# Kernel optimization log

Hardware: AMD Instinct MI355X
Metric: run time of the kernel (lower is better)

Reference implementation:

```python
import jax, jax.numpy as jnp
import numpy as np

D_MODEL = 2048
NUM_HEADS = 16
D_K = D_MODEL // NUM_HEADS


def setup_inputs() -> dict:
    key = jax.random.key(0)
    ks = jax.random.split(key, 9)
    s = 1.0 / np.sqrt(D_MODEL)
    x = jax.random.normal(ks[0], (4, 4096, D_MODEL), dtype=jnp.float32)
    wq = jax.random.uniform(ks[1], (D_MODEL, D_MODEL), jnp.float32, -s, s)
    bq = jax.random.uniform(ks[2], (D_MODEL,), jnp.float32, -s, s)
    wk = jax.random.uniform(ks[3], (D_MODEL, D_MODEL), jnp.float32, -s, s)
    bk = jax.random.uniform(ks[4], (D_MODEL,), jnp.float32, -s, s)
    wv = jax.random.uniform(ks[5], (D_MODEL, D_MODEL), jnp.float32, -s, s)
    bv = jax.random.uniform(ks[6], (D_MODEL,), jnp.float32, -s, s)
    wo = jax.random.uniform(ks[7], (D_MODEL, D_MODEL), jnp.float32, -s, s)
    bo = jax.random.uniform(ks[8], (D_MODEL,), jnp.float32, -s, s)
    return {"x": x, "wq": wq, "bq": bq, "wk": wk, "bk": bk,
            "wv": wv, "bv": bv, "wo": wo, "bo": bo}


def _heads(t, B, S):
    # (B, S, d_model) -> (B, H, S, d_k)
    return t.reshape(B, S, NUM_HEADS, D_K).transpose(0, 2, 1, 3)


def reference(x, wq, bq, wk, bk, wv, bv, wo, bo):
    B, S, _ = x.shape
    Q = _heads(x @ wq.T + bq, B, S)
    K = _heads(x @ wk.T + bk, B, S)
    V = _heads(x @ wv.T + bv, B, S)
    # elu(x)+1 feature map
    Q = jax.nn.elu(Q) + 1.0
    K = jax.nn.elu(K) + 1.0
    # KV: (B,H,d_k,d_k)
    KV = jnp.einsum('bhsd,bhse->bhde', K, V)
    QKV = jnp.einsum('bhsd,bhde->bhse', Q, KV)
    K_sum = jnp.sum(K, axis=-2)                      # (B,H,d_k)
    QK_sum = jnp.einsum('bhsd,bhd->bhs', Q, K_sum)   # (B,H,S)
    out = QKV / (QK_sum[..., None] + 1e-8)
    out = out.transpose(0, 2, 1, 3).reshape(B, S, D_MODEL)
    return out @ wo.T + bo
```

## Files before the change

kernel.cpp:

```cpp
#include <hip/hip_runtime.h>


#define D_MODEL 2048
#define SEQ     4096
#define BATCH   4
#define HEADS   16
#define DKH     128
#define M_TOK   16384
#define NBH     64

using frag8 = __attribute__((ext_vector_type(8))) short;
using f32x4 = __attribute__((ext_vector_type(4))) float;

typedef __attribute__((address_space(1))) const unsigned int g_u32;
typedef __attribute__((address_space(3))) unsigned int       l_u32;

__device__ __forceinline__ unsigned short f2bf(float f) {
  unsigned u = __float_as_uint(f);
  u = u + 0x7fffu + ((u >> 16) & 1u);
  return (unsigned short)(u >> 16);
}
__device__ __forceinline__ float bf2f(unsigned short h) {
  return __uint_as_float(((unsigned)h) << 16);
}

__global__ __launch_bounds__(256) void convert_f2bf_kernel(
    const float* __restrict__ in, unsigned short* __restrict__ out, int n4) {
  int i = blockIdx.x * 256 + threadIdx.x;
  if (i < n4) {
    float4 v = reinterpret_cast<const float4*>(in)[i];
    ushort4 o;
    o.x = f2bf(v.x); o.y = f2bf(v.y); o.z = f2bf(v.z); o.w = f2bf(v.w);
    reinterpret_cast<ushort4*>(out)[i] = o;
  }
}


#define ST_B(GB, LD, SLOT, KC)                                                \
  _Pragma("unroll") for (int j_ = 0; j_ < 2; ++j_)                            \
    __builtin_amdgcn_global_load_lds(                                         \
        (g_u32*)((GB) + (srow + wid * 16 + j_ * 8 + (lane >> 3)) * (LD)       \
                 + (KC) + scg * 8),                                           \
        (l_u32*)(sh + (SLOT) * 16384 + 8192 + (wid * 16 + j_ * 8) * 64),      \
        16, 0, 0);

#define ST_A(GA, LD, SP, ST, KC)                                              \
    __builtin_amdgcn_global_load_lds(                                         \
        (g_u32*)((GA) + (srow + (ST) * 32 + (wid & 3) * 8 + (lane >> 3)) * (LD) \
                 + (KC) + (wid >> 2) * 32 + scg * 8),                         \
        (l_u32*)(sh + ((SP) + (wid >> 2)) * 16384 +                           \
                 ((ST) * 32 + (wid & 3) * 8) * 64),                           \
        16, 0, 0);

#define RD_A(S0, S1, Q)                                                       \
  a0[0] = *(const frag8*)(lds + (S0) * 16384 + tA + (Q) * 2048);              \
  a0[1] = *(const frag8*)(lds + (S0) * 16384 + tA + (Q) * 2048 + 1024);       \
  a1[0] = *(const frag8*)(lds + (S1) * 16384 + tA + (Q) * 2048);              \
  a1[1] = *(const frag8*)(lds + (S1) * 16384 + tA + (Q) * 2048 + 1024);

#define RD_B(D0, D1, S0, S1)                                                  \
  _Pragma("unroll") for (int n_ = 0; n_ < 4; ++n_) {                          \
    D0[n_] = *(const frag8*)(lds + (S0) * 16384 + tB + n_ * 1024);            \
    D1[n_] = *(const frag8*)(lds + (S1) * 16384 + tB + n_ * 1024);            \
  }

#define MM8(AQ, B0, B1)                                                       \
  __builtin_amdgcn_s_setprio(1);                                              \
  _Pragma("unroll") for (int j_ = 0; j_ < 2; ++j_)                            \
  _Pragma("unroll") for (int n_ = 0; n_ < 4; ++n_)                            \
    acc[(AQ) + j_][n_] = __builtin_amdgcn_mfma_f32_16x16x32_bf16(             \
        a0[j_], B0[n_], acc[(AQ) + j_][n_], 0, 0, 0);                         \
  _Pragma("unroll") for (int j_ = 0; j_ < 2; ++j_)                            \
  _Pragma("unroll") for (int n_ = 0; n_ < 4; ++n_)                            \
    acc[(AQ) + j_][n_] = __builtin_amdgcn_mfma_f32_16x16x32_bf16(             \
        a1[j_], B1[n_], acc[(AQ) + j_][n_], 0, 0, 0);                         \
  __builtin_amdgcn_s_setprio(0);

#define BAR __builtin_amdgcn_s_barrier()
#define LG0                                                                   \
  asm volatile("s_waitcnt lgkmcnt(0)" ::: "memory");                          \
  __builtin_amdgcn_sched_barrier(0)

template <int MODE, bool XMAJOR>
__global__ __launch_bounds__(512, 2) void gemm256_nt_kernel(
    const unsigned short* __restrict__ A, long lda,
    const unsigned short* __restrict__ Bm, long ldb,
    void* __restrict__ Cv, long ldc,
    const float* __restrict__ bias, float* __restrict__ aux, int K) {
  __shared__ unsigned short sh[65536];
  const int lane = threadIdx.x & 63, wid = threadIdx.x >> 6;
  const int wm = wid >> 2, wn = wid & 3;
  const int lr = lane & 15, lh = lane >> 4;

  const int gx = gridDim.x, gy = gridDim.y;
  const int cpx = (gx * gy) >> 3;
  const int P = blockIdx.y * gx + blockIdx.x;
  const int Lw = (P & 7) * cpx + (P >> 3);
  int bx, by;
  if (XMAJOR) { bx = Lw / gy; by = Lw - bx * gy; }
  else        { by = Lw / gx; bx = Lw - by * gx; }

  const long m0 = (long)by * 256, n0 = (long)bx * 256;
  const unsigned short* Ablk = A + m0 * lda;
  const unsigned short* Bblk = Bm + n0 * ldb;
  const int NT = K >> 6;

  const int qA = (wm * 4 + lh) ^ (lr & 7);
  const int qB = ((wn >> 1) * 4 + lh) ^ (lr & 7);
  const unsigned short* lds = sh;
  const int tA = lr * 64 + qA * 8;
  const int tB = 8192 + ((wn & 1) * 64 + lr) * 64 + qB * 8;

  const int sqd = (lane & 7) ^ (lane >> 3);
  const int scg = sqd & 3;
  const long srow = (long)((sqd >> 2) * 128);

  f32x4 acc[8][4];
#pragma unroll
  for (int m = 0; m < 8; ++m)
#pragma unroll
    for (int n = 0; n < 4; ++n) acc[m][n] = (f32x4){0.f, 0.f, 0.f, 0.f};

  frag8 a0[2], a1[2], bu0[4], bu1[4], bv0[4], bv1[4];

  ST_B(Bblk, ldb, 0, 0)
  ST_B(Bblk, ldb, 1, 32)
  ST_A(Ablk, lda, 0, 0, 0) ST_A(Ablk, lda, 0, 1, 0)
  ST_A(Ablk, lda, 0, 2, 0) ST_A(Ablk, lda, 0, 3, 0)
  if (NT > 1) {
    ST_B(Bblk, ldb, 2, 64)
    ST_B(Bblk, ldb, 3, 96)
    ST_A(Ablk, lda, 2, 0, 64) ST_A(Ablk, lda, 2, 1, 64)
  }
  asm volatile("s_waitcnt vmcnt(6)" ::: "memory");
  BAR;

  const int NI = NT >> 1;
  for (int i = 0; i < NI; ++i) {
    const int kv = i * 128 + 64, kw = i * 128 + 128, kx = i * 128 + 192;
    const bool wok = (i + 1) < NI;
    RD_A(0, 1, 0)
    RD_B(bu0, bu1, 0, 1)
    ST_A(Ablk, lda, 2, 2, kv) ST_A(Ablk, lda, 2, 3, kv)
    asm volatile("s_waitcnt lgkmcnt(8)" ::: "memory");
    BAR; LG0;
    MM8(0, bu0, bu1)
    BAR;
    RD_A(0, 1, 1)
    if (wok) { ST_B(Bblk, ldb, 0, kw) }
    BAR; LG0;
    MM8(2, bu0, bu1)
    BAR;
    RD_A(0, 1, 2)
    if (wok) { ST_B(Bblk, ldb, 1, kw + 32) }
    BAR; LG0;
    MM8(4, bu0, bu1)
    BAR;
    RD_A(0, 1, 3)
    if (wok) { ST_A(Ablk, lda, 0, 0, kw) ST_A(Ablk, lda, 0, 1, kw) }
    if (wok) asm volatile("s_waitcnt vmcnt(6)" ::: "memory");
    else     asm volatile("s_waitcnt vmcnt(0)" ::: "memory");
    BAR; LG0;
    MM8(6, bu0, bu1)
    BAR;
    RD_A(2, 3, 0)
    RD_B(bv0, bv1, 2, 3)
    if (wok) { ST_A(Ablk, lda, 0, 2, kw) ST_A(Ablk, lda, 0, 3, kw) }
    asm volatile("s_waitcnt lgkmcnt(8)" ::: "memory");
    BAR; LG0;
    MM8(0, bv0, bv1)
    BAR;
    RD_A(2, 3, 1)
    if (wok) { ST_B(Bblk, ldb, 2, kx) }
    BAR; LG0;
    MM8(2, bv0, bv1)
    BAR;
    RD_A(2, 3, 2)
    if (wok) { ST_B(Bblk, ldb, 3, kx + 32) }
    BAR; LG0;
    MM8(4, bv0, bv1)
    BAR;
    RD_A(2, 3, 3)
    if (wok) { ST_A(Ablk, lda, 2, 0, kx) ST_A(Ablk, lda, 2, 1, kx)
               asm volatile("s_waitcnt vmcnt(6)" ::: "memory"); }
    BAR; LG0;
    MM8(6, bv0, bv1)
    BAR;
  }

  if constexpr (MODE == 1) {
    __shared__ float red2[256];
    if (threadIdx.x < 256) red2[threadIdx.x] = 0.f;
    __syncthreads();
#pragma unroll
    for (int m = 0; m < 8; ++m)
#pragma unroll
      for (int r = 0; r < 4; ++r) {
        const int lrow = wm * 128 + (m >> 1) * 32 + (m & 1) * 16 + lh * 4 + r;
        const long row = m0 + lrow;
        float part = 0.f;
#pragma unroll
        for (int n = 0; n < 4; ++n) {
          long col = n0 + wn * 64 + n * 16 + lr;
          float v = acc[m][n][r] + bias[row];
          v = v > 0.f ? v + 1.f : __expf(v);
          unsigned short us = f2bf(v);
          ((unsigned short*)Cv)[row * ldc + col] = us;
          part += bf2f(us);
        }
#pragma unroll
        for (int s = 1; s < 16; s <<= 1) part += __shfl_xor(part, s);
        if (lr == 0) atomicAdd(&red2[lrow], part);
      }
    __syncthreads();
    if (threadIdx.x < 256)
      atomicAdd(&aux[(n0 >> 12) * 2048 + m0 + threadIdx.x], red2[threadIdx.x]);
  } else {
#pragma unroll
    for (int m = 0; m < 8; ++m)
#pragma unroll
      for (int n = 0; n < 4; ++n)
#pragma unroll
        for (int r = 0; r < 4; ++r) {
          long row = m0 + wm * 128 + (m >> 1) * 32 + (m & 1) * 16 + lh * 4 + r;
          long col = n0 + wn * 64 + n * 16 + lr;
          float v = acc[m][n][r];
          if (MODE == 0) {
            v += bias[col]; v = v > 0.f ? v + 1.f : __expf(v);
            ((unsigned short*)Cv)[row * ldc + col] = f2bf(v);
          } else if (MODE == 2) {
            v += bias[row];
            ((unsigned short*)Cv)[row * ldc + col] = f2bf(v);
          } else {
            v += bias[col];
            ((float*)Cv)[row * ldc + col] = v;
          }
        }
  }
}

__device__ __forceinline__ void stage_tile(const unsigned short* __restrict__ G,
                                           long ld, unsigned short* __restrict__ L) {
  const int w = threadIdx.x >> 6, l = threadIdx.x & 63;
#pragma unroll
  for (int r = 0; r < 4; ++r) {
    const int chunk = w * 4 + r;
    const int row = chunk * 8 + (l >> 3);
    const int col = (l & 7) * 8;
    __builtin_amdgcn_global_load_lds((g_u32*)(G + (long)row * ld + col),
                                     (l_u32*)(L + chunk * 512), 16, 0, 0);
  }
}

__device__ __forceinline__ void gemm_mainloop(const unsigned short* __restrict__ A, long lda,
                                              const unsigned short* __restrict__ B, long ldb,
                                              int K, unsigned short* lA, unsigned short* lB,
                                              f32x4 acc[4][4]) {
  const int lane = threadIdx.x & 63;
  const int wid  = threadIdx.x >> 6;
  const int wr = wid >> 1, wc = wid & 1;
  const int lr = lane & 15, lh = lane >> 4;
  for (int k0 = 0; k0 < K; k0 += 64) {
    stage_tile(A + k0, lda, lA);
    stage_tile(B + k0, ldb, lB);
    __syncthreads();
#pragma unroll
    for (int kk = 0; kk < 64; kk += 32) {
      frag8 av[4], bv[4];
#pragma unroll
      for (int m = 0; m < 4; ++m)
        av[m] = *reinterpret_cast<const frag8*>(lA + (wr * 64 + m * 16 + lr) * 64 + kk + lh * 8);
#pragma unroll
      for (int n = 0; n < 4; ++n)
        bv[n] = *reinterpret_cast<const frag8*>(lB + (wc * 64 + n * 16 + lr) * 64 + kk + lh * 8);
#pragma unroll
      for (int m = 0; m < 4; ++m)
#pragma unroll
        for (int n = 0; n < 4; ++n)
          acc[m][n] = __builtin_amdgcn_mfma_f32_16x16x32_bf16(av[m], bv[n], acc[m][n], 0, 0, 0);
    }
    __syncthreads();
  }
}

#define ACC_INIT(acc)                                   \
  _Pragma("unroll") for (int m_ = 0; m_ < 4; ++m_)      \
  _Pragma("unroll") for (int n_ = 0; n_ < 4; ++n_)      \
      acc[m_][n_] = (f32x4){0.f, 0.f, 0.f, 0.f};

__global__ __launch_bounds__(256) void kvt_partial_kernel(
    const unsigned short* __restrict__ VT, const unsigned short* __restrict__ KT,
    float* __restrict__ part) {
  __shared__ unsigned short lA[128 * 64], lB[128 * 64];
  const int z = blockIdx.x;
  const int bh = z >> 3, c = z & 7;
  const int b = bh >> 4, h = bh & 15;
  const long tOff = (long)b * SEQ + (long)c * 512;
  const unsigned short* A  = VT + (long)(h * DKH) * M_TOK + tOff;
  const unsigned short* Bm = KT + (long)(h * DKH) * M_TOK + tOff;
  f32x4 acc[4][4];
  ACC_INIT(acc);
  gemm_mainloop(A, M_TOK, Bm, M_TOK, 512, lA, lB, acc);
  const int lane = threadIdx.x & 63, wid = threadIdx.x >> 6;
  const int wr = wid >> 1, wc = wid & 1, lr = lane & 15, lh = lane >> 4;
  float* out = part + (long)z * (DKH * DKH);
#pragma unroll
  for (int m = 0; m < 4; ++m)
#pragma unroll
    for (int n = 0; n < 4; ++n)
#pragma unroll
      for (int r = 0; r < 4; ++r) {
        int row = wr * 64 + m * 16 + lh * 4 + r;
        int col = wc * 64 + n * 16 + lr;
        out[row * DKH + col] = acc[m][n][r];
      }
}

__global__ __launch_bounds__(256) void reduce_kvt_kernel(
    const float* __restrict__ part, unsigned short* __restrict__ kvt) {
  int i = blockIdx.x * 256 + threadIdx.x;
  if (i < NBH * DKH * DKH) {
    int bh = i >> 14, j = i & 16383;
    float s = 0.f;
#pragma unroll
    for (int c = 0; c < 8; ++c) s += part[(((long)bh * 8 + c) << 14) + j];
    kvt[i] = f2bf(s);
  }
}

__global__ __launch_bounds__(256) void qkv_kernel(const unsigned short* __restrict__ Q,
                                                  const unsigned short* __restrict__ KVT,
                                                  const float* __restrict__ ksum,
                                                  unsigned short* __restrict__ attn) {
  __shared__ unsigned short lA[128 * 64], lB[128 * 64];
  __shared__ float qs[128];
  const int z = blockIdx.z, b = z >> 4, h = z & 15;
  const long m0 = (long)blockIdx.y * 128;
  const unsigned short* A  = Q + ((long)b * SEQ + m0) * D_MODEL + h * DKH;
  const unsigned short* Bm = KVT + (long)z * (DKH * DKH);
  const float* ks = ksum + (long)b * 2048 + h * DKH;
  f32x4 acc[4][4];
  ACC_INIT(acc);
  const int lane = threadIdx.x & 63, wid = threadIdx.x >> 6;
  const int wr = wid >> 1, wc = wid & 1, lr = lane & 15, lh = lane >> 4;
  const int qrow = threadIdx.x >> 1, qhalf = threadIdx.x & 1;
  float qacc = 0.f;
  for (int k0 = 0; k0 < DKH; k0 += 64) {
    stage_tile(A + k0, D_MODEL, lA);
    stage_tile(Bm + k0, DKH, lB);
    __syncthreads();
    {
      const unsigned* pr = (const unsigned*)(lA + qrow * 64 + qhalf * 32);
      const float* kk = ks + k0 + qhalf * 32;
#pragma unroll
      for (int j = 0; j < 16; ++j) {
        unsigned u = pr[j];
        qacc += bf2f((unsigned short)(u & 0xffff)) * kk[2 * j] +
                bf2f((unsigned short)(u >> 16)) * kk[2 * j + 1];
      }
    }
#pragma unroll
    for (int kk2 = 0; kk2 < 64; kk2 += 32) {
      frag8 av[4], bv[4];
#pragma unroll
      for (int m = 0; m < 4; ++m)
        av[m] = *reinterpret_cast<const frag8*>(lA + (wr * 64 + m * 16 + lr) * 64 + kk2 + lh * 8);
#pragma unroll
      for (int n = 0; n < 4; ++n)
        bv[n] = *reinterpret_cast<const frag8*>(lB + (wc * 64 + n * 16 + lr) * 64 + kk2 + lh * 8);
#pragma unroll
      for (int m = 0; m < 4; ++m)
#pragma unroll
        for (int n = 0; n < 4; ++n)
          acc[m][n] = __builtin_amdgcn_mfma_f32_16x16x32_bf16(av[m], bv[n], acc[m][n], 0, 0, 0);
    }
    __syncthreads();
  }
  qacc += __shfl_xor(qacc, 1);
  if (qhalf == 0) qs[qrow] = qacc;
  __syncthreads();
#pragma unroll
  for (int m = 0; m < 4; ++m)
#pragma unroll
    for (int n = 0; n < 4; ++n)
#pragma unroll
      for (int r = 0; r < 4; ++r) {
        const int lrow = wr * 64 + m * 16 + lh * 4 + r;
        long row = m0 + lrow;
        int  col = wc * 64 + n * 16 + lr;
        float dnm = qs[lrow] + 1e-8f;
        float v = acc[m][n][r] / dnm;
        attn[((long)b * SEQ + row) * D_MODEL + h * DKH + col] = f2bf(v);
      }
}

#define OFF_XB   0L
#define OFF_WQ   (OFF_XB + (long)M_TOK * D_MODEL * 2)
#define OFF_WK   (OFF_WQ + (long)D_MODEL * D_MODEL * 2)
#define OFF_WV   (OFF_WK + (long)D_MODEL * D_MODEL * 2)
#define OFF_WO   (OFF_WV + (long)D_MODEL * D_MODEL * 2)
#define OFF_QB   (OFF_WO + (long)D_MODEL * D_MODEL * 2)
#define OFF_KT   (OFF_QB + (long)M_TOK * D_MODEL * 2)
#define OFF_VT   (OFF_KT + (long)M_TOK * D_MODEL * 2)
#define OFF_PART (OFF_VT + (long)M_TOK * D_MODEL * 2)
#define OFF_KVT  (OFF_PART + (long)512 * DKH * DKH * 4)
#define OFF_KSUM (OFF_KVT + (long)NBH * DKH * DKH * 2)
#define OFF_QSUM (OFF_KSUM + (long)NBH * DKH * 4)
#define OFF_ATTN OFF_XB

extern "C" void kernel_launch(void* const* d_in, const int* in_sizes, int n_in,
                              void* d_out, int out_size, void* d_ws, size_t ws_size,
                              hipStream_t stream) {
  const float* x  = (const float*)d_in[0];
  const float* wq = (const float*)d_in[1];
  const float* bq = (const float*)d_in[2];
  const float* wk = (const float*)d_in[3];
  const float* bk = (const float*)d_in[4];
  const float* wv = (const float*)d_in[5];
  const float* bv = (const float*)d_in[6];
  const float* wo = (const float*)d_in[7];
  const float* bo = (const float*)d_in[8];

  char* ws = (char*)d_ws;
  unsigned short* xb   = (unsigned short*)(ws + OFF_XB);
  unsigned short* wqb  = (unsigned short*)(ws + OFF_WQ);
  unsigned short* wkb  = (unsigned short*)(ws + OFF_WK);
  unsigned short* wvb  = (unsigned short*)(ws + OFF_WV);
  unsigned short* wob  = (unsigned short*)(ws + OFF_WO);
  unsigned short* Qb   = (unsigned short*)(ws + OFF_QB);
  unsigned short* KTb  = (unsigned short*)(ws + OFF_KT);
  unsigned short* VTb  = (unsigned short*)(ws + OFF_VT);
  float*          part = (float*)(ws + OFF_PART);
  unsigned short* KVTb = (unsigned short*)(ws + OFF_KVT);
  float*          ksum = (float*)(ws + OFF_KSUM);
  unsigned short* attn = (unsigned short*)(ws + OFF_ATTN);

  dim3 blk(256);
  dim3 blk5(512);

  convert_f2bf_kernel<<<(M_TOK * D_MODEL / 4) / 256, blk, 0, stream>>>(x, xb, M_TOK * D_MODEL / 4);
  convert_f2bf_kernel<<<(D_MODEL * D_MODEL / 4) / 256, blk, 0, stream>>>(wq, wqb, D_MODEL * D_MODEL / 4);
  convert_f2bf_kernel<<<(D_MODEL * D_MODEL / 4) / 256, blk, 0, stream>>>(wk, wkb, D_MODEL * D_MODEL / 4);
  convert_f2bf_kernel<<<(D_MODEL * D_MODEL / 4) / 256, blk, 0, stream>>>(wv, wvb, D_MODEL * D_MODEL / 4);
  convert_f2bf_kernel<<<(D_MODEL * D_MODEL / 4) / 256, blk, 0, stream>>>(wo, wob, D_MODEL * D_MODEL / 4);

  hipMemsetAsync(ksum, 0, NBH * DKH * sizeof(float), stream);

  gemm256_nt_kernel<0, false><<<dim3(D_MODEL / 256, M_TOK / 256), blk5, 0, stream>>>(
      xb, D_MODEL, wqb, D_MODEL, Qb, D_MODEL, bq, nullptr, D_MODEL);
  gemm256_nt_kernel<1, true><<<dim3(M_TOK / 256, D_MODEL / 256), blk5, 0, stream>>>(
      wkb, D_MODEL, xb, D_MODEL, KTb, M_TOK, bk, ksum, D_MODEL);
  gemm256_nt_kernel<2, true><<<dim3(M_TOK / 256, D_MODEL / 256), blk5, 0, stream>>>(
      wvb, D_MODEL, xb, D_MODEL, VTb, M_TOK, bv, nullptr, D_MODEL);

  kvt_partial_kernel<<<512, blk, 0, stream>>>(VTb, KTb, part);
  reduce_kvt_kernel<<<(NBH * DKH * DKH) / 256, blk, 0, stream>>>(part, KVTb);

  qkv_kernel<<<dim3(1, SEQ / 128, NBH), blk, 0, stream>>>(Qb, KVTb, ksum, attn);

  gemm256_nt_kernel<3, false><<<dim3(D_MODEL / 256, M_TOK / 256), blk5, 0, stream>>>(
      attn, D_MODEL, wob, D_MODEL, d_out, D_MODEL, bo, nullptr, D_MODEL);
}
```

Baseline: 662.7 us.

## Fuse conversion launches and reuse staged KV tile across four row tiles

The five fp32-to-bf16 conversion launches become one kernel that picks its source buffer from the block index, removing four launches. The qkv kernel now stages the full 128x128 KV^T tile into shared memory once per block and loops over four 128-row Q tiles, so the KV matrix is reloaded less often and the grid is four times smaller. Shared memory use doubles and each block runs longer, which lowers the number of blocks available to fill the CUs.

```diff
diff --git a/kernel.cpp b/kernel.cpp
--- a/kernel.cpp
+++ b/kernel.cpp
@@ -24,15 +24,31 @@
   return __uint_as_float(((unsigned)h) << 16);
 }
 
-__global__ __launch_bounds__(256) void convert_f2bf_kernel(
-    const float* __restrict__ in, unsigned short* __restrict__ out, int n4) {
-  int i = blockIdx.x * 256 + threadIdx.x;
-  if (i < n4) {
-    float4 v = reinterpret_cast<const float4*>(in)[i];
-    ushort4 o;
-    o.x = f2bf(v.x); o.y = f2bf(v.y); o.z = f2bf(v.z); o.w = f2bf(v.w);
-    reinterpret_cast<ushort4*>(out)[i] = o;
-  }
+__global__ __launch_bounds__(256) void convert_all_kernel(
+    const float* __restrict__ x,  const float* __restrict__ wq,
+    const float* __restrict__ wk, const float* __restrict__ wv,
+    const float* __restrict__ wo,
+    unsigned short* __restrict__ xb,  unsigned short* __restrict__ wqb,
+    unsigned short* __restrict__ wkb, unsigned short* __restrict__ wvb,
+    unsigned short* __restrict__ wob) {
+  const int bb = blockIdx.x;
+  const float* in;
+  unsigned short* out;
+  long i;
+  if (bb < 32768) {
+    in = x; out = xb; i = (long)bb * 256 + threadIdx.x;
+  } else {
+    const int t = bb - 32768, s = t >> 12, r = t & 4095;
+    i = (long)r * 256 + threadIdx.x;
+    if (s == 0)      { in = wq; out = wqb; }
+    else if (s == 1) { in = wk; out = wkb; }
+    else if (s == 2) { in = wv; out = wvb; }
+    else             { in = wo; out = wob; }
+  }
+  float4 v = reinterpret_cast<const float4*>(in)[i];
+  ushort4 o;
+  o.x = f2bf(v.x); o.y = f2bf(v.y); o.z = f2bf(v.z); o.w = f2bf(v.w);
+  reinterpret_cast<ushort4*>(out)[i] = o;
 }
 
 
@@ -332,66 +348,71 @@
                                                   const unsigned short* __restrict__ KVT,
                                                   const float* __restrict__ ksum,
                                                   unsigned short* __restrict__ attn) {
-  __shared__ unsigned short lA[128 * 64], lB[128 * 64];
+  __shared__ unsigned short lA[2][128 * 64], lB[2][128 * 64];
   __shared__ float qs[128];
-  const int z = blockIdx.z, b = z >> 4, h = z & 15;
-  const long m0 = (long)blockIdx.y * 128;
-  const unsigned short* A  = Q + ((long)b * SEQ + m0) * D_MODEL + h * DKH;
+  const int z = blockIdx.y, b = z >> 4, h = z & 15;
+  const long mbase = (long)blockIdx.x * 512;
   const unsigned short* Bm = KVT + (long)z * (DKH * DKH);
   const float* ks = ksum + (long)b * 2048 + h * DKH;
-  f32x4 acc[4][4];
-  ACC_INIT(acc);
   const int lane = threadIdx.x & 63, wid = threadIdx.x >> 6;
   const int wr = wid >> 1, wc = wid & 1, lr = lane & 15, lh = lane >> 4;
   const int qrow = threadIdx.x >> 1, qhalf = threadIdx.x & 1;
-  float qacc = 0.f;
-  for (int k0 = 0; k0 < DKH; k0 += 64) {
-    stage_tile(A + k0, D_MODEL, lA);
-    stage_tile(Bm + k0, DKH, lB);
-    __syncthreads();
+
+  stage_tile(Bm,      DKH, lB[0]);
+  stage_tile(Bm + 64, DKH, lB[1]);
+
+  for (int mt = 0; mt < 4; ++mt) {
+    const unsigned short* A = Q + ((long)b * SEQ + mbase + mt * 128) * D_MODEL + h * DKH;
+    stage_tile(A,      D_MODEL, lA[0]);
+    stage_tile(A + 64, D_MODEL, lA[1]);
+    __syncthreads();
+    float qacc = 0.f;
     {
-      const unsigned* pr = (const unsigned*)(lA + qrow * 64 + qhalf * 32);
-      const float* kk = ks + k0 + qhalf * 32;
-#pragma unroll
-      for (int j = 0; j < 16; ++j) {
+      const unsigned* pr = (const unsigned*)(lA[qhalf] + qrow * 64);
+      const float* kk = ks + qhalf * 64;
+#pragma unroll
+      for (int j = 0; j < 32; ++j) {
         unsigned u = pr[j];
         qacc += bf2f((unsigned short)(u & 0xffff)) * kk[2 * j] +
                 bf2f((unsigned short)(u >> 16)) * kk[2 * j + 1];
       }
     }
-#pragma unroll
-    for (int kk2 = 0; kk2 < 64; kk2 += 32) {
-      frag8 av[4], bv[4];
-#pragma unroll
-      for (int m = 0; m < 4; ++m)
-        av[m] = *reinterpret_cast<const frag8*>(lA + (wr * 64 + m * 16 + lr) * 64 + kk2 + lh * 8);
+    qacc += __shfl_xor(qacc, 1);
+    if (qhalf == 0) qs[qrow] = qacc;
+    f32x4 acc[4][4];
+    ACC_INIT(acc);
+#pragma unroll
+    for (int hf = 0; hf < 2; ++hf)
+#pragma unroll
+      for (int kk2 = 0; kk2 < 64; kk2 += 32) {
+        frag8 av[4], bv[4];
+#pragma unroll
+        for (int m = 0; m < 4; ++m)
+          av[m] = *reinterpret_cast<const frag8*>(lA[hf] + (wr * 64 + m * 16 + lr) * 64 + kk2 + lh * 8);
+#pragma unroll
+        for (int n = 0; n < 4; ++n)
+          bv[n] = *reinterpret_cast<const frag8*>(lB[hf] + (wc * 64 + n * 16 + lr) * 64 + kk2 + lh * 8);
+#pragma unroll
+        for (int m = 0; m < 4; ++m)
+#pragma unroll
+          for (int n = 0; n < 4; ++n)
+            acc[m][n] = __builtin_amdgcn_mfma_f32_16x16x32_bf16(av[m], bv[n], acc[m][n], 0, 0, 0);
+      }
+    __syncthreads();
+#pragma unroll
+    for (int m = 0; m < 4; ++m)
 #pragma unroll
       for (int n = 0; n < 4; ++n)
-        bv[n] = *reinterpret_cast<const frag8*>(lB + (wc * 64 + n * 16 + lr) * 64 + kk2 + lh * 8);
-#pragma unroll
-      for (int m = 0; m < 4; ++m)
-#pragma unroll
-        for (int n = 0; n < 4; ++n)
-          acc[m][n] = __builtin_amdgcn_mfma_f32_16x16x32_bf16(av[m], bv[n], acc[m][n], 0, 0, 0);
-    }
-    __syncthreads();
-  }
-  qacc += __shfl_xor(qacc, 1);
-  if (qhalf == 0) qs[qrow] = qacc;
-  __syncthreads();
-#pragma unroll
-  for (int m = 0; m < 4; ++m)
-#pragma unroll
-    for (int n = 0; n < 4; ++n)
-#pragma unroll
-      for (int r = 0; r < 4; ++r) {
-        const int lrow = wr * 64 + m * 16 + lh * 4 + r;
-        long row = m0 + lrow;
-        int  col = wc * 64 + n * 16 + lr;
-        float dnm = qs[lrow] + 1e-8f;
-        float v = acc[m][n][r] / dnm;
-        attn[((long)b * SEQ + row) * D_MODEL + h * DKH + col] = f2bf(v);
-      }
+#pragma unroll
+        for (int r = 0; r < 4; ++r) {
+          const int lrow = wr * 64 + m * 16 + lh * 4 + r;
+          const long row = mbase + mt * 128 + lrow;
+          const int col = wc * 64 + n * 16 + lr;
+          float dnm = qs[lrow] + 1e-8f;
+          float v = acc[m][n][r] / dnm;
+          attn[((long)b * SEQ + row) * D_MODEL + h * DKH + col] = f2bf(v);
+        }
+  }
 }
 
 #define OFF_XB   0L
@@ -438,11 +459,8 @@
   dim3 blk(256);
   dim3 blk5(512);
 
-  convert_f2bf_kernel<<<(M_TOK * D_MODEL / 4) / 256, blk, 0, stream>>>(x, xb, M_TOK * D_MODEL / 4);
-  convert_f2bf_kernel<<<(D_MODEL * D_MODEL / 4) / 256, blk, 0, stream>>>(wq, wqb, D_MODEL * D_MODEL / 4);
-  convert_f2bf_kernel<<<(D_MODEL * D_MODEL / 4) / 256, blk, 0, stream>>>(wk, wkb, D_MODEL * D_MODEL / 4);
-  convert_f2bf_kernel<<<(D_MODEL * D_MODEL / 4) / 256, blk, 0, stream>>>(wv, wvb, D_MODEL * D_MODEL / 4);
-  convert_f2bf_kernel<<<(D_MODEL * D_MODEL / 4) / 256, blk, 0, stream>>>(wo, wob, D_MODEL * D_MODEL / 4);
+  convert_all_kernel<<<49152, blk, 0, stream>>>(x, wq, wk, wv, wo,
+                                                xb, wqb, wkb, wvb, wob);
 
   hipMemsetAsync(ksum, 0, NBH * DKH * sizeof(float), stream);
 
@@ -456,7 +474,7 @@
   kvt_partial_kernel<<<512, blk, 0, stream>>>(VTb, KTb, part);
   reduce_kvt_kernel<<<(NBH * DKH * DKH) / 256, blk, 0, stream>>>(part, KVTb);
 
-  qkv_kernel<<<dim3(1, SEQ / 128, NBH), blk, 0, stream>>>(Qb, KVTb, ksum, attn);
+  qkv_kernel<<<dim3(SEQ / 512, NBH), blk, 0, stream>>>(Qb, KVTb, ksum, attn);
 
   gemm256_nt_kernel<3, false><<<dim3(D_MODEL / 256, M_TOK / 256), blk5, 0, stream>>>(
       attn, D_MODEL, wob, D_MODEL, d_out, D_MODEL, bo, nullptr, D_MODEL);
```

After: 653.3 us, median of 2. About the same (-1.4%).
